# Performance work log

Hardware: AMD Instinct MI355X
Metric: run time of the kernel (lower is better)

The kernel has to match this reference:

```python
import jax, jax.numpy as jnp
import numpy as np

N, E, G = 50000, 800000, 64
NODE_DIM, HID, HEADS, EDGE_DIM = 128, 256, 4, 2
LAYER_IN = [NODE_DIM, HID, HID]
LAYER_HEADS = [HEADS, HEADS, 1]
BN_EPS = 1e-5


def setup_inputs() -> dict:
    key = jax.random.key(0)
    ks = iter(jax.random.split(key, 80))
    def nrm(shape, s=0.05):
        return jax.random.normal(next(ks), shape, jnp.float32) * s
    inp = {}
    inp['x'] = jax.random.normal(next(ks), (N, NODE_DIM), jnp.float32)
    inp['edge_index'] = jax.random.randint(next(ks), (2, E), 0, N, jnp.int32)
    inp['edge_attr'] = jax.random.normal(next(ks), (E, EDGE_DIM), jnp.float32)
    inp['batch'] = jnp.sort(jax.random.randint(next(ks), (N,), 0, G, jnp.int32))
    for i in range(3):
        H = LAYER_HEADS[i]; C = HID // H
        inp[f'W{i}'] = nrm((LAYER_IN[i], H * C))
        inp[f'asrc{i}'] = nrm((H, C))
        inp[f'adst{i}'] = nrm((H, C))
        inp[f'We{i}'] = nrm((EDGE_DIM, H * C))
        inp[f'aedge{i}'] = nrm((H, C))
        inp[f'bconv{i}'] = jnp.zeros((HID,), jnp.float32)
        inp[f'bn{i}_g'] = jnp.ones((HID,), jnp.float32)
        inp[f'bn{i}_b'] = jnp.zeros((HID,), jnp.float32)
        inp[f'bn{i}_m'] = nrm((HID,), 0.01)
        inp[f'bn{i}_v'] = jnp.ones((HID,), jnp.float32)
    inp['Wskip'] = nrm((NODE_DIM, HID))
    inp['bskip'] = jnp.zeros((HID,), jnp.float32)
    inp['Wp1'] = nrm((2 * HID, HID))
    inp['bp1'] = jnp.zeros((HID,), jnp.float32)
    inp['Wp2'] = nrm((HID, 1))
    inp['bp2'] = jnp.zeros((1,), jnp.float32)
    return inp


def gat_conv(x, src, dst, ea, W, a_s, a_d, We, a_e, b, H, concat):
    n = x.shape[0]
    C = W.shape[1] // H
    h = (x @ W).reshape(n, H, C)                      # [N,H,C]
    # attention logits per edge (src/dst node terms + edge term)
    al = ((h * a_s).sum(-1)[src]
          + (h * a_d).sum(-1)[dst]
          + ((ea @ We).reshape(-1, H, C) * a_e).sum(-1))  # [Et,H]
    al = jax.nn.leaky_relu(al, 0.2)
    # segment softmax over destination nodes
    amax = jax.ops.segment_max(al, dst, num_segments=n)
    ex = jnp.exp(al - amax[dst])
    den = jax.ops.segment_sum(ex, dst, num_segments=n)
    alpha = ex / (den[dst] + 1e-16)
    out = jax.ops.segment_sum(h[src] * alpha[..., None], dst, num_segments=n)  # [N,H,C]
    out = out.reshape(n, H * C) if concat else out.mean(axis=1)
    return out + b


def _forward(x, edge_index, edge_attr, batch, layer_params, Wskip, bskip, Wp1, bp1, Wp2, bp2):
    n = x.shape[0]
    # add self-loops (PyG GATConv default), edge_attr filled with mean
    loop = jnp.arange(n, dtype=edge_index.dtype)
    src = jnp.concatenate([edge_index[0], loop])
    dst = jnp.concatenate([edge_index[1], loop])
    ea = jnp.concatenate([edge_attr, jnp.broadcast_to(edge_attr.mean(0), (n, edge_attr.shape[1]))], axis=0)
    identity = x
    for i, (W, a_s, a_d, We, a_e, b, g, be, rm, rv) in enumerate(layer_params):
        layer_identity = (identity @ Wskip + bskip) if i == 0 else identity
        concat = i < 2
        H = LAYER_HEADS[i]
        h = gat_conv(x, src, dst, ea, W, a_s, a_d, We, a_e, b, H, concat)
        h = (h - rm) * jax.lax.rsqrt(rv + BN_EPS) * g + be   # BatchNorm1d (eval)
        h = jax.nn.elu(h)
        x = h + layer_identity
        identity = x
    # global mean + max pool per graph
    counts = jnp.maximum(jax.ops.segment_sum(jnp.ones((n,), x.dtype), batch, num_segments=G), 1.0)
    mean_pool = jax.ops.segment_sum(x, batch, num_segments=G) / counts[:, None]
    max_pool = jax.ops.segment_max(x, batch, num_segments=G)
    emb = jnp.concatenate([mean_pool, max_pool], axis=1)      # [G, 2*HID]
    hmid = jax.nn.relu(emb @ Wp1 + bp1)
    return hmid @ Wp2 + bp2                                   # [G, 1]


def reference(x, edge_index, edge_attr, batch,
              W0, asrc0, adst0, We0, aedge0, bconv0, bn0_g, bn0_b, bn0_m, bn0_v,
              W1, asrc1, adst1, We1, aedge1, bconv1, bn1_g, bn1_b, bn1_m, bn1_v,
              W2, asrc2, adst2, We2, aedge2, bconv2, bn2_g, bn2_b, bn2_m, bn2_v,
              Wskip, bskip, Wp1, bp1, Wp2, bp2):
    layer_params = [
        (W0, asrc0, adst0, We0, aedge0, bconv0, bn0_g, bn0_b, bn0_m, bn0_v),
        (W1, asrc1, adst1, We1, aedge1, bconv1, bn1_g, bn1_b, bn1_m, bn1_v),
        (W2, asrc2, adst2, We2, aedge2, bconv2, bn2_g, bn2_b, bn2_m, bn2_v),
    ]
    return _forward(x, edge_index, edge_attr, batch, layer_params, Wskip, bskip, Wp1, bp1, Wp2, bp2)
```

## Files before the change

### kernel.cpp

```cpp
#include <hip/hip_runtime.h>
#include <cfloat>

#define Nn 50000
#define Ee 800000
#define Etot (Ee + Nn)
#define Gg 64
#define HIDc 256
#define BN_EPS 1e-5f

typedef unsigned int   uint32;
typedef unsigned short ushort16;
typedef short  bf16x8 __attribute__((ext_vector_type(8)));
typedef float  f32x4  __attribute__((ext_vector_type(4)));

__device__ inline ushort16 f2bf(float f) {
    uint32 u = __float_as_uint(f);
    u = (u + 0x7fffu + ((u >> 16) & 1u)) >> 16;
    return (ushort16)u;
}
__device__ inline uint32 pack2(float a, float b) {
    return (uint32)f2bf(a) | ((uint32)f2bf(b) << 16);
}
__device__ inline uint32 fenc(float f) {
    uint32 b = __float_as_uint(f);
    return (b & 0x80000000u) ? ~b : (b | 0x80000000u);
}
__device__ inline float fdec(uint32 u) {
    uint32 b = (u & 0x80000000u) ? (u & 0x7fffffffu) : ~u;
    return __uint_as_float(b);
}

__device__ inline long ws_index(int c, int k, int KB) {
    int cb = c >> 4, m = c & 15, kb = k >> 5, q = (k >> 3) & 3, e = k & 7;
    return (((long)(cb * KB + kb) * 64 + q * 16 + m) << 3) + e;
}

#define CVT4 (Nn * 128 / 4)
#define CVT_BLKS ((CVT4 + 255) / 256)
#define EBKS ((Etot + 255) / 256)
__global__ __launch_bounds__(256) void prep_kernel(
        const float* __restrict__ ea, float* __restrict__ ea_s,
        const float* __restrict__ We0, const float* __restrict__ ae0,
        const float* __restrict__ We1, const float* __restrict__ ae1,
        const float* __restrict__ We2, const float* __restrict__ ae2,
        float* __restrict__ M,
        const float* __restrict__ W0, const float* __restrict__ Wskip,
        const float* __restrict__ W1, const float* __restrict__ W2,
        ushort16* __restrict__ WtC, ushort16* __restrict__ Wt1,
        ushort16* __restrict__ Wt2,
        const float* __restrict__ x, ushort16* __restrict__ xbf,
        const int* __restrict__ ei, int* __restrict__ counts) {
    int bid = blockIdx.x, t = threadIdx.x;
    if (bid < 256) {
        __shared__ float sh0[256], sh1[256];
        float s0 = 0.f, s1 = 0.f;
        for (int e = bid * 256 + t; e < Ee; e += 256 * 256) {
            s0 += ea[2 * e];
            s1 += ea[2 * e + 1];
        }
        sh0[t] = s0; sh1[t] = s1;
        __syncthreads();
        for (int off = 128; off > 0; off >>= 1) {
            if (t < off) { sh0[t] += sh0[t + off]; sh1[t] += sh1[t + off]; }
            __syncthreads();
        }
        if (t == 0) { atomicAdd(&ea_s[0], sh0[0]); atomicAdd(&ea_s[1], sh1[0]); }
    } else if (bid == 256) {
        if (t >= 18) return;
        int l = t < 8 ? 0 : (t < 16 ? 1 : 2);
        int r = t - l * 8;
        const float* We = (l == 0) ? We0 : (l == 1 ? We1 : We2);
        const float* ae = (l == 0) ? ae0 : (l == 1 ? ae1 : ae2);
        int Hl = (l < 2) ? 4 : 1;
        int Cl = 256 / Hl;
        int d = r / Hl, hh = r % Hl;
        float s = 0.f;
        for (int c = 0; c < Cl; ++c)
            s += We[d * 256 + hh * Cl + c] * ae[hh * Cl + c];
        M[l * 8 + r] = s;
    } else if (bid < 385) {
        int k = bid - 257;
        WtC[ws_index(t, k, 4)] = f2bf(W0[(long)k * 256 + t]);
    } else if (bid < 513) {
        int k = bid - 385;
        WtC[ws_index(256 + t, k, 4)] = f2bf(Wskip[(long)k * 256 + t]);
    } else if (bid < 769) {
        int k = bid - 513;
        Wt1[ws_index(t, k, 8)] = f2bf(W1[(long)k * 256 + t]);
    } else if (bid < 1025) {
        int k = bid - 769;
        Wt2[ws_index(t, k, 8)] = f2bf(W2[(long)k * 256 + t]);
    } else if (bid < 1025 + CVT_BLKS) {
        int i = (bid - 1025) * 256 + t;
        if (i < CVT4) {
            float4 v = *(const float4*)&x[i * 4];
            ushort4 o;
            o.x = f2bf(v.x); o.y = f2bf(v.y); o.z = f2bf(v.z); o.w = f2bf(v.w);
            *(ushort4*)&xbf[i * 4] = o;
        }
    } else {
        int e = (bid - 1025 - CVT_BLKS) * 256 + t;
        if (e < Etot) {
            int d = (e < Ee) ? ei[Ee + e] : (e - Ee);
            atomicAdd(&counts[d], 1);
        }
    }
}

__global__ void scan1_kernel(const int* __restrict__ in, int* __restrict__ inc,
                             int* __restrict__ bsums) {
    __shared__ int sh[256];
    int i = blockIdx.x * 256 + threadIdx.x;
    int v = (i < Nn) ? in[i] : 0;
    sh[threadIdx.x] = v;
    __syncthreads();
    for (int off = 1; off < 256; off <<= 1) {
        int t = ((int)threadIdx.x >= off) ? sh[threadIdx.x - off] : 0;
        __syncthreads();
        sh[threadIdx.x] += t;
        __syncthreads();
    }
    if (i < Nn) inc[i] = sh[threadIdx.x];
    if (threadIdx.x == 255) bsums[blockIdx.x] = sh[255];
}

__global__ void scan23_kernel(const int* __restrict__ inc, const int* __restrict__ bsums,
                              int* __restrict__ row_start, int* __restrict__ cursor, int nb) {
    __shared__ int sh[256];
    int b = blockIdx.x, t = threadIdx.x;
    sh[t] = (t < b && t < nb) ? bsums[t] : 0;
    __syncthreads();
    for (int off = 128; off > 0; off >>= 1) {
        if (t < off) sh[t] += sh[t + off];
        __syncthreads();
    }
    int base = sh[0];
    int i = b * 256 + t;
    if (i < Nn) {
        int v = inc[i] + base;
        row_start[i + 1] = v;
        cursor[i + 1] = v;
    }
    if (i == 0) { row_start[0] = 0; cursor[0] = 0; }
}

__global__ void scatter_kernel(const int* __restrict__ ei, const float* __restrict__ ea,
                               const float* __restrict__ ea_sum, int* __restrict__ cursor,
                               int* __restrict__ src_sorted, float* __restrict__ ea_sorted) {
    int e = blockIdx.x * blockDim.x + threadIdx.x;
    if (e >= Etot) return;
    int s, d; float e0, e1;
    if (e < Ee) {
        s = ei[e]; d = ei[Ee + e];
        e0 = ea[2 * e]; e1 = ea[2 * e + 1];
    } else {
        s = d = e - Ee;
        const float invE = 1.f / (float)Ee;
        e0 = ea_sum[0] * invE; e1 = ea_sum[1] * invE;
    }
    int pos = atomicAdd(&cursor[d], 1);
    src_sorted[pos] = s;
    ea_sorted[2 * pos]     = e0;
    ea_sorted[2 * pos + 1] = e1;
}

#define LDK 40
__global__ __launch_bounds__(256) void mfma_gemm_kernel(
        const ushort16* __restrict__ A,
        const ushort16* __restrict__ WS,
        uint32* __restrict__ outF,
        uint32* __restrict__ outS,
        const float* __restrict__ bskip,
        const float* __restrict__ a_s, const float* __restrict__ a_d,
        float* __restrict__ ssrc, float* __restrict__ sdst,
        int n, int K) {
    __shared__ ushort16 As[128 * LDK];
    const int t    = threadIdx.x;
    const int row0 = blockIdx.x * 128;
    const int c0   = blockIdx.y * 128;
    const bool isSkip = (outS != nullptr) && (c0 >= 256);
    const int cc0  = isSkip ? c0 - 256 : c0;
    const int wave = t >> 6, lane = t & 63;
    const int wr = wave >> 1, wc = wave & 1;
    const int l15 = lane & 15, quad = lane >> 4;
    const int KB = K >> 5;

    f32x4 acc[4][4];
#pragma unroll
    for (int j = 0; j < 4; ++j)
#pragma unroll
        for (int i = 0; i < 4; ++i) {
            acc[j][i][0] = 0.f; acc[j][i][1] = 0.f;
            acc[j][i][2] = 0.f; acc[j][i][3] = 0.f;
        }

    const int sm = t & 127;
    const int so = t >> 7;

    for (int k0 = 0; k0 < K; k0 += 32) {
        const int kb = k0 >> 5;
#pragma unroll
        for (int h = 0; h < 2; ++h) {
            int oct = so + 2 * h;
            int grow = row0 + sm;
            uint4 va = make_uint4(0, 0, 0, 0);
            if (grow < n) va = *(const uint4*)&A[(long)grow * K + k0 + 8 * oct];
            *(uint4*)&As[sm * LDK + 8 * oct] = va;
        }
        bf16x8 bfv[4];
#pragma unroll
        for (int j = 0; j < 4; ++j) {
            int cb = ((c0 + wc * 64) >> 4) + j;
            bfv[j] = *(const bf16x8*)&WS[(((long)cb * KB + kb) * 64 + lane) << 3];
        }
        __syncthreads();
        bf16x8 af[4];
#pragma unroll
        for (int i = 0; i < 4; ++i)
            af[i] = *(const bf16x8*)&As[(wr * 64 + i * 16 + l15) * LDK + quad * 8];
#pragma unroll
        for (int j = 0; j < 4; ++j)
#pragma unroll
            for (int i = 0; i < 4; ++i)
                acc[j][i] = __builtin_amdgcn_mfma_f32_16x16x32_bf16(
                    bfv[j], af[i], acc[j][i], 0, 0, 0);
        __syncthreads();
    }

    float4 bb[4];
#pragma unroll
    for (int j = 0; j < 4; ++j) {
        if (isSkip) bb[j] = *(const float4*)&bskip[cc0 + wc * 64 + j * 16 + quad * 4];
        else        bb[j] = make_float4(0.f, 0.f, 0.f, 0.f);
    }

    uint32* tgt = isSkip ? outS : outF;
#pragma unroll
    for (int i = 0; i < 4; ++i) {
        int row = row0 + wr * 64 + i * 16 + l15;
        if (row >= n) continue;
#pragma unroll
        for (int j = 0; j < 4; ++j) {
            int col = cc0 + wc * 64 + j * 16 + quad * 4;
            uint2 pk;
            pk.x = pack2(acc[j][i][0] + bb[j].x, acc[j][i][1] + bb[j].y);
            pk.y = pack2(acc[j][i][2] + bb[j].z, acc[j][i][3] + bb[j].w);
            *(uint2*)&tgt[(long)row * 128 + (col >> 1)] = pk;
        }
    }

    if (!isSkip && a_s != nullptr) {
        float4 asv[4], adv[4];
#pragma unroll
        for (int j = 0; j < 4; ++j) {
            int col = cc0 + wc * 64 + j * 16 + quad * 4;
            asv[j] = *(const float4*)&a_s[col];
            adv[j] = *(const float4*)&a_d[col];
        }
        const int part = (cc0 + wc * 64) >> 6;
#pragma unroll
        for (int i = 0; i < 4; ++i) {
            float ps = 0.f, pd = 0.f;
#pragma unroll
            for (int j = 0; j < 4; ++j) {
                ps += acc[j][i][0] * asv[j].x + acc[j][i][1] * asv[j].y
                    + acc[j][i][2] * asv[j].z + acc[j][i][3] * asv[j].w;
                pd += acc[j][i][0] * adv[j].x + acc[j][i][1] * adv[j].y
                    + acc[j][i][2] * adv[j].z + acc[j][i][3] * adv[j].w;
            }
            ps += __shfl_xor(ps, 16); ps += __shfl_xor(ps, 32);
            pd += __shfl_xor(pd, 16); pd += __shfl_xor(pd, 32);
            if (quad == 0) {
                int row = row0 + wr * 64 + i * 16 + l15;
                if (row < n) {
                    ssrc[row * 4 + part] = ps;
                    sdst[row * 4 + part] = pd;
                }
            }
        }
    }
}

template <int H>
__global__ __launch_bounds__(256) void edge_softmax_kernel(
        const int* __restrict__ src_sorted, const int* __restrict__ row_start,
        const float* __restrict__ ea_sorted, const float* __restrict__ ssrc,
        const float* __restrict__ sdst, const float* __restrict__ M,
        float* __restrict__ w) {
    int node = (blockIdx.x * blockDim.x + threadIdx.x) >> 4;
    int l16 = threadIdx.x & 15;
    if (node >= Nn) return;
    int beg = row_start[node], end = row_start[node + 1];
    int deg = end - beg;
    float sd[H], M0[H], M1[H], m[H], den[H];
    if (H == 4) {
#pragma unroll
        for (int h = 0; h < H; ++h) sd[h] = sdst[node * 4 + h];
    } else {
        float4 v = *(const float4*)&sdst[node * 4];
        sd[0] = v.x + v.y + v.z + v.w;
    }
#pragma unroll
    for (int h = 0; h < H; ++h) {
        M0[h] = M[h]; M1[h] = M[H + h];
        m[h] = -FLT_MAX; den[h] = 0.f;
    }
    auto ssval = [&](int s, int h) -> float {
        if (H == 4) return ssrc[s * 4 + h];
        float4 v = *(const float4*)&ssrc[s * 4];
        return v.x + v.y + v.z + v.w;
    };
    if (deg <= 64) {
        float lreg[4][H];
#pragma unroll
        for (int k = 0; k < 4; ++k) {
            int idx = beg + l16 + (k << 4);
            if (idx < end) {
                int s = src_sorted[idx];
                float e0 = ea_sorted[2 * idx], e1 = ea_sorted[2 * idx + 1];
#pragma unroll
                for (int h = 0; h < H; ++h) {
                    float l = ssval(s, h) + sd[h] + e0 * M0[h] + e1 * M1[h];
                    l = (l > 0.f) ? l : 0.2f * l;
                    lreg[k][h] = l;
                    if (l > m[h]) { den[h] = den[h] * __expf(m[h] - l) + 1.f; m[h] = l; }
                    else den[h] += __expf(l - m[h]);
                }
            }
        }
#pragma unroll
        for (int h = 0; h < H; ++h) {
#pragma unroll
            for (int off = 1; off < 16; off <<= 1) {
                float om = __shfl_xor(m[h], off);
                float od = __shfl_xor(den[h], off);
                float nm = fmaxf(m[h], om);
                den[h] = den[h] * __expf(m[h] - nm) + od * __expf(om - nm);
                m[h] = nm;
            }
            den[h] = 1.f / (den[h] + 1e-16f);
        }
#pragma unroll
        for (int k = 0; k < 4; ++k) {
            int idx = beg + l16 + (k << 4);
            if (idx < end) {
#pragma unroll
                for (int h = 0; h < H; ++h)
                    w[(long)idx * H + h] = __expf(lreg[k][h] - m[h]) * den[h];
            }
        }
    } else {
        for (int idx = beg + l16; idx < end; idx += 16) {
            int s = src_sorted[idx];
            float e0 = ea_sorted[2 * idx], e1 = ea_sorted[2 * idx + 1];
#pragma unroll
            for (int h = 0; h < H; ++h) {
                float l = ssval(s, h) + sd[h] + e0 * M0[h] + e1 * M1[h];
                l = (l > 0.f) ? l : 0.2f * l;
                w[(long)idx * H + h] = l;
                if (l > m[h]) { den[h] = den[h] * __expf(m[h] - l) + 1.f; m[h] = l; }
                else den[h] += __expf(l - m[h]);
            }
        }
#pragma unroll
        for (int h = 0; h < H; ++h) {
#pragma unroll
            for (int off = 1; off < 16; off <<= 1) {
                float om = __shfl_xor(m[h], off);
                float od = __shfl_xor(den[h], off);
                float nm = fmaxf(m[h], om);
                den[h] = den[h] * __expf(m[h] - nm) + od * __expf(om - nm);
                m[h] = nm;
            }
            den[h] = 1.f / (den[h] + 1e-16f);
        }
        for (int idx = beg + l16; idx < end; idx += 16) {
#pragma unroll
            for (int h = 0; h < H; ++h) {
                float l = w[(long)idx * H + h];
                w[(long)idx * H + h] = __expf(l - m[h]) * den[h];
            }
        }
    }
}

template <int H>
__global__ __launch_bounds__(256) void agg_kernel(
        const int* __restrict__ src_sorted, const int* __restrict__ row_start,
        const uint32* __restrict__ hbuf2, const float* __restrict__ w,
        const float* __restrict__ bconv,
        const float* __restrict__ bn_g, const float* __restrict__ bn_b,
        const float* __restrict__ bn_m, const float* __restrict__ bn_v,
        const uint32* __restrict__ identity2, uint32* __restrict__ out2) {
    int wv = threadIdx.x >> 6;
    int l  = threadIdx.x & 63;
    int node = blockIdx.x * 4 + wv;
    if (node >= Nn) return;
    const int hh = (l >> 4) & (H - 1);
    const int l15 = l & 15, gbase = l & 48;
    int beg = row_start[node], end = row_start[node + 1];
    float a0 = 0.f, a1 = 0.f, a2 = 0.f, a3 = 0.f;
    for (int base = beg; base < end; base += 16) {
        int bi  = base + l15;
        int bic = min(bi, end - 1);
        int sp  = src_sorted[bic];
        float wp = (bi < end) ? w[(long)bic * H + hh] : 0.f;
        uint2 f[16];
        float wk[16];
#pragma unroll
        for (int k = 0; k < 16; ++k) {
            int sl = gbase + k;
            int sk = __shfl(sp, sl, 64);
            wk[k]  = __shfl(wp, sl, 64);
            f[k] = *(const uint2*)&hbuf2[(long)sk * 128 + 2 * l];
        }
#pragma unroll
        for (int k = 0; k < 16; ++k) {
            float ww = wk[k];
            a0 += ww * __uint_as_float(f[k].x << 16);
            a1 += ww * __uint_as_float(f[k].x & 0xffff0000u);
            a2 += ww * __uint_as_float(f[k].y << 16);
            a3 += ww * __uint_as_float(f[k].y & 0xffff0000u);
        }
    }
    int c = 4 * l;
    float4 bcv = *(const float4*)&bconv[c];
    float4 bgv = *(const float4*)&bn_g[c];
    float4 bbv = *(const float4*)&bn_b[c];
    float4 bmv = *(const float4*)&bn_m[c];
    float4 bvv = *(const float4*)&bn_v[c];
    float v0 = a0 + bcv.x, v1 = a1 + bcv.y, v2 = a2 + bcv.z, v3 = a3 + bcv.w;
    v0 = (v0 - bmv.x) * rsqrtf(bvv.x + BN_EPS) * bgv.x + bbv.x;
    v1 = (v1 - bmv.y) * rsqrtf(bvv.y + BN_EPS) * bgv.y + bbv.y;
    v2 = (v2 - bmv.z) * rsqrtf(bvv.z + BN_EPS) * bgv.z + bbv.z;
    v3 = (v3 - bmv.w) * rsqrtf(bvv.w + BN_EPS) * bgv.w + bbv.w;
    v0 = (v0 > 0.f) ? v0 : (expf(v0) - 1.f);
    v1 = (v1 > 0.f) ? v1 : (expf(v1) - 1.f);
    v2 = (v2 > 0.f) ? v2 : (expf(v2) - 1.f);
    v3 = (v3 > 0.f) ? v3 : (expf(v3) - 1.f);
    uint2 idu = *(const uint2*)&identity2[(long)node * 128 + 2 * l];
    v0 += __uint_as_float(idu.x << 16);
    v1 += __uint_as_float(idu.x & 0xffff0000u);
    v2 += __uint_as_float(idu.y << 16);
    v3 += __uint_as_float(idu.y & 0xffff0000u);
    uint2 o;
    o.x = pack2(v0, v1);
    o.y = pack2(v2, v3);
    *(uint2*)&out2[(long)node * 128 + 2 * l] = o;
}

#define POOL_ROWS 32
__global__ __launch_bounds__(128) void pool_kernel(
        const uint32* __restrict__ x2, const int* __restrict__ batch,
        float* __restrict__ psum, uint32* __restrict__ pmax, float* __restrict__ pcnt) {
    int c2 = threadIdx.x;
    int n0 = blockIdx.x * POOL_ROWS;
    if (n0 >= Nn) return;
    int n1 = min(n0 + POOL_ROWS, Nn);
    int cur = batch[n0];
    float s0 = 0.f, s1 = 0.f, m0 = -FLT_MAX, m1 = -FLT_MAX;
    int cnt = 0;
    int c = 2 * c2;
    for (int i = n0; i < n1; ++i) {
        int g = batch[i];
        if (g != cur) {
            atomicAdd(&psum[cur * 256 + c], s0);
            atomicAdd(&psum[cur * 256 + c + 1], s1);
            atomicMax(&pmax[cur * 256 + c], fenc(m0));
            atomicMax(&pmax[cur * 256 + c + 1], fenc(m1));
            if (c2 == 0) atomicAdd(&pcnt[cur], (float)cnt);
            cur = g; s0 = s1 = 0.f; m0 = m1 = -FLT_MAX; cnt = 0;
        }
        uint32 u = x2[(long)i * 128 + c2];
        float lo = __uint_as_float(u << 16);
        float hi = __uint_as_float(u & 0xffff0000u);
        s0 += lo; s1 += hi;
        m0 = fmaxf(m0, lo); m1 = fmaxf(m1, hi);
        ++cnt;
    }
    atomicAdd(&psum[cur * 256 + c], s0);
    atomicAdd(&psum[cur * 256 + c + 1], s1);
    atomicMax(&pmax[cur * 256 + c], fenc(m0));
    atomicMax(&pmax[cur * 256 + c + 1], fenc(m1));
    if (c2 == 0) atomicAdd(&pcnt[cur], (float)cnt);
}

__global__ __launch_bounds__(256) void mlp_kernel(
        const float* __restrict__ psum, const uint32* __restrict__ pmax,
        const float* __restrict__ pcnt, const float* __restrict__ Wp1,
        const float* __restrict__ bp1, const float* __restrict__ Wp2,
        const float* __restrict__ bp2, float* __restrict__ out) {
    int g = blockIdx.x;
    int j = threadIdx.x;
    float inv = 1.f / fmaxf(pcnt[g], 1.f);
    float acc = bp1[j];
    for (int k = 0; k < 256; ++k)
        acc += (psum[g * 256 + k] * inv) * Wp1[k * 256 + j];
    for (int k = 0; k < 256; ++k)
        acc += fdec(pmax[g * 256 + k]) * Wp1[(256 + k) * 256 + j];
    float v = fmaxf(acc, 0.f) * Wp2[j];
    __shared__ float red[256];
    red[j] = v;
    __syncthreads();
    for (int off = 128; off > 0; off >>= 1) {
        if (j < off) red[j] += red[j + off];
        __syncthreads();
    }
    if (j == 0) out[g] = red[0] + bp2[0];
}

extern "C" void kernel_launch(void* const* d_in, const int* in_sizes, int n_in,
                              void* d_out, int out_size, void* d_ws, size_t ws_size,
                              hipStream_t stream) {
    const float* x   = (const float*)d_in[0];
    const int*   ei  = (const int*)d_in[1];
    const float* ea  = (const float*)d_in[2];
    const int*   bat = (const int*)d_in[3];
    auto LP = [&](int l, int j) { return (const float*)d_in[4 + l * 10 + j]; };
    const float* Wskip = (const float*)d_in[34];
    const float* bskip = (const float*)d_in[35];
    const float* Wp1   = (const float*)d_in[36];
    const float* bp1   = (const float*)d_in[37];
    const float* Wp2   = (const float*)d_in[38];
    const float* bp2   = (const float*)d_in[39];
    float* out = (float*)d_out;

    char* p = (char*)d_ws;
    auto alloc = [&](size_t bytes) { void* r = (void*)p; p += (bytes + 255) & ~(size_t)255; return r; };
    uint32*   hbuf2  = (uint32*)alloc((size_t)Nn * 256 * 2);
    uint32*   skipbf = (uint32*)alloc((size_t)Nn * 128 * 4);
    uint32*   resA   = (uint32*)alloc((size_t)Nn * 128 * 4);
    uint32*   resB   = (uint32*)alloc((size_t)Nn * 128 * 4);
    ushort16* xbf    = (ushort16*)alloc((size_t)Nn * 128 * 2);
    float*    wbuf   = (float*)alloc((size_t)Etot * 4 * 4);
    float*    ea_sorted = (float*)alloc((size_t)Etot * 2 * 4);
    float*    ssrc   = (float*)alloc((size_t)Nn * 4 * 4);
    float*    sdst   = (float*)alloc((size_t)Nn * 4 * 4);
    int*      counts = (int*)alloc((size_t)Nn * 4);
    int*      incb   = (int*)alloc((size_t)Nn * 4);
    int*      row_start = (int*)alloc((size_t)(Nn + 1) * 4);
    int*      cursor    = (int*)alloc((size_t)(Nn + 1) * 4);
    int*      src_sorted = (int*)alloc((size_t)Etot * 4);
    int*      bsums  = (int*)alloc(256 * 4);
    float*    ea_s   = (float*)alloc(2 * 4);
    float*    Mbuf   = (float*)alloc(32 * 4);
    ushort16* WtC    = (ushort16*)alloc((size_t)512 * 128 * 2);
    ushort16* Wt1    = (ushort16*)alloc((size_t)256 * 256 * 2);
    ushort16* Wt2    = (ushort16*)alloc((size_t)256 * 256 * 2);
    float*    psum   = (float*)alloc((size_t)Gg * 256 * 4);
    uint32*   pmax   = (uint32*)alloc((size_t)Gg * 256 * 4);
    float*    pcnt   = (float*)alloc((size_t)Gg * 4);

    const int nb = (Nn + 255) / 256;
    const int sgrid = (Nn * 16 + 255) / 256;

    hipMemsetAsync(counts, 0, (size_t)Nn * 4, stream);
    hipMemsetAsync(ea_s, 0, 8, stream);
    hipMemsetAsync(psum, 0, (size_t)Gg * 256 * 4 * 2 + (size_t)Gg * 4, stream);

    prep_kernel<<<1025 + CVT_BLKS + EBKS, 256, 0, stream>>>(
        ea, ea_s, LP(0,3), LP(0,4), LP(1,3), LP(1,4), LP(2,3), LP(2,4), Mbuf,
        LP(0,0), Wskip, LP(1,0), LP(2,0), WtC, Wt1, Wt2, x, xbf, ei, counts);

    scan1_kernel<<<nb, 256, 0, stream>>>(counts, incb, bsums);
    scan23_kernel<<<nb, 256, 0, stream>>>(incb, bsums, row_start, cursor, nb);
    scatter_kernel<<<EBKS, 256, 0, stream>>>(ei, ea, ea_s, cursor, src_sorted, ea_sorted);

    {
        dim3 g0((Nn + 127) / 128, 4);
        mfma_gemm_kernel<<<g0, 256, 0, stream>>>(
            xbf, WtC, hbuf2, skipbf, bskip,
            LP(0,1), LP(0,2), ssrc, sdst, Nn, 128);
    }

    const uint32* lid[3] = { skipbf, resA, resB };
    uint32*       lou[3] = { resA, resB, resA };
    const ushort16* lain[3] = { nullptr, (ushort16*)resA, (ushort16*)resB };
    const ushort16* lwt[3]  = { nullptr, Wt1, Wt2 };
    for (int l = 0; l < 3; ++l) {
        if (l > 0) {
            dim3 gl((Nn + 127) / 128, 2);
            mfma_gemm_kernel<<<gl, 256, 0, stream>>>(
                lain[l], lwt[l], hbuf2, nullptr, nullptr,
                LP(l,1), LP(l,2), ssrc, sdst, Nn, 256);
        }
        if (l < 2) {
            edge_softmax_kernel<4><<<sgrid, 256, 0, stream>>>(
                src_sorted, row_start, ea_sorted, ssrc, sdst, Mbuf + l * 8, wbuf);
            agg_kernel<4><<<(Nn + 3) / 4, 256, 0, stream>>>(src_sorted, row_start, hbuf2, wbuf,
                LP(l,5), LP(l,6), LP(l,7), LP(l,8), LP(l,9), lid[l], lou[l]);
        } else {
            edge_softmax_kernel<1><<<sgrid, 256, 0, stream>>>(
                src_sorted, row_start, ea_sorted, ssrc, sdst, Mbuf + l * 8, wbuf);
            agg_kernel<1><<<(Nn + 3) / 4, 256, 0, stream>>>(src_sorted, row_start, hbuf2, wbuf,
                LP(l,5), LP(l,6), LP(l,7), LP(l,8), LP(l,9), lid[l], lou[l]);
        }
    }

    pool_kernel<<<(Nn + POOL_ROWS - 1) / POOL_ROWS, 128, 0, stream>>>(resA, bat, psum, pmax, pcnt);
    mlp_kernel<<<Gg, 256, 0, stream>>>(psum, pmax, pcnt, Wp1, bp1, Wp2, bp2, out);
}
```

Baseline: 643.7 us.

## Fuse edge softmax into the aggregation kernel using per-wave shared memory

```diff
diff --git a/kernel.cpp b/kernel.cpp
--- a/kernel.cpp
+++ b/kernel.cpp
@@ -282,147 +282,144 @@
 }
 
 template <int H>
-__global__ __launch_bounds__(256) void edge_softmax_kernel(
+__global__ __launch_bounds__(256) void agg_fused_kernel(
         const int* __restrict__ src_sorted, const int* __restrict__ row_start,
         const float* __restrict__ ea_sorted, const float* __restrict__ ssrc,
         const float* __restrict__ sdst, const float* __restrict__ M,
-        float* __restrict__ w) {
-    int node = (blockIdx.x * blockDim.x + threadIdx.x) >> 4;
-    int l16 = threadIdx.x & 15;
-    if (node >= Nn) return;
-    int beg = row_start[node], end = row_start[node + 1];
-    int deg = end - beg;
-    float sd[H], M0[H], M1[H], m[H], den[H];
-    if (H == 4) {
-#pragma unroll
-        for (int h = 0; h < H; ++h) sd[h] = sdst[node * 4 + h];
-    } else {
-        float4 v = *(const float4*)&sdst[node * 4];
-        sd[0] = v.x + v.y + v.z + v.w;
-    }
-#pragma unroll
-    for (int h = 0; h < H; ++h) {
-        M0[h] = M[h]; M1[h] = M[H + h];
-        m[h] = -FLT_MAX; den[h] = 0.f;
-    }
-    auto ssval = [&](int s, int h) -> float {
-        if (H == 4) return ssrc[s * 4 + h];
-        float4 v = *(const float4*)&ssrc[s * 4];
-        return v.x + v.y + v.z + v.w;
-    };
-    if (deg <= 64) {
-        float lreg[4][H];
-#pragma unroll
-        for (int k = 0; k < 4; ++k) {
-            int idx = beg + l16 + (k << 4);
-            if (idx < end) {
-                int s = src_sorted[idx];
-                float e0 = ea_sorted[2 * idx], e1 = ea_sorted[2 * idx + 1];
-#pragma unroll
-                for (int h = 0; h < H; ++h) {
-                    float l = ssval(s, h) + sd[h] + e0 * M0[h] + e1 * M1[h];
-                    l = (l > 0.f) ? l : 0.2f * l;
-                    lreg[k][h] = l;
-                    if (l > m[h]) { den[h] = den[h] * __expf(m[h] - l) + 1.f; m[h] = l; }
-                    else den[h] += __expf(l - m[h]);
-                }
-            }
-        }
-#pragma unroll
-        for (int h = 0; h < H; ++h) {
-#pragma unroll
-            for (int off = 1; off < 16; off <<= 1) {
-                float om = __shfl_xor(m[h], off);
-                float od = __shfl_xor(den[h], off);
-                float nm = fmaxf(m[h], om);
-                den[h] = den[h] * __expf(m[h] - nm) + od * __expf(om - nm);
-                m[h] = nm;
-            }
-            den[h] = 1.f / (den[h] + 1e-16f);
-        }
-#pragma unroll
-        for (int k = 0; k < 4; ++k) {
-            int idx = beg + l16 + (k << 4);
-            if (idx < end) {
-#pragma unroll
-                for (int h = 0; h < H; ++h)
-                    w[(long)idx * H + h] = __expf(lreg[k][h] - m[h]) * den[h];
-            }
-        }
-    } else {
-        for (int idx = beg + l16; idx < end; idx += 16) {
-            int s = src_sorted[idx];
-            float e0 = ea_sorted[2 * idx], e1 = ea_sorted[2 * idx + 1];
-#pragma unroll
-            for (int h = 0; h < H; ++h) {
-                float l = ssval(s, h) + sd[h] + e0 * M0[h] + e1 * M1[h];
-                l = (l > 0.f) ? l : 0.2f * l;
-                w[(long)idx * H + h] = l;
-                if (l > m[h]) { den[h] = den[h] * __expf(m[h] - l) + 1.f; m[h] = l; }
-                else den[h] += __expf(l - m[h]);
-            }
-        }
-#pragma unroll
-        for (int h = 0; h < H; ++h) {
-#pragma unroll
-            for (int off = 1; off < 16; off <<= 1) {
-                float om = __shfl_xor(m[h], off);
-                float od = __shfl_xor(den[h], off);
-                float nm = fmaxf(m[h], om);
-                den[h] = den[h] * __expf(m[h] - nm) + od * __expf(om - nm);
-                m[h] = nm;
-            }
-            den[h] = 1.f / (den[h] + 1e-16f);
-        }
-        for (int idx = beg + l16; idx < end; idx += 16) {
-#pragma unroll
-            for (int h = 0; h < H; ++h) {
-                float l = w[(long)idx * H + h];
-                w[(long)idx * H + h] = __expf(l - m[h]) * den[h];
-            }
-        }
-    }
-}
-
-template <int H>
-__global__ __launch_bounds__(256) void agg_kernel(
-        const int* __restrict__ src_sorted, const int* __restrict__ row_start,
-        const uint32* __restrict__ hbuf2, const float* __restrict__ w,
+        const uint32* __restrict__ hbuf2,
         const float* __restrict__ bconv,
         const float* __restrict__ bn_g, const float* __restrict__ bn_b,
         const float* __restrict__ bn_m, const float* __restrict__ bn_v,
-        const uint32* __restrict__ identity2, uint32* __restrict__ out2) {
-    int wv = threadIdx.x >> 6;
-    int l  = threadIdx.x & 63;
-    int node = blockIdx.x * 4 + wv;
+        const uint32* __restrict__ identity2, uint32* __restrict__ out2,
+        float* __restrict__ wspill) {
+    __shared__ int   s_sh[4][64];
+    __shared__ float w_sh[4][64 * H];
+    const int wv = threadIdx.x >> 6;
+    const int l  = threadIdx.x & 63;
+    const int node = blockIdx.x * 4 + wv;
     if (node >= Nn) return;
-    const int hh = (l >> 4) & (H - 1);
-    const int l15 = l & 15, gbase = l & 48;
-    int beg = row_start[node], end = row_start[node + 1];
+    const int hh = (H == 4) ? (l >> 4) : 0;
+    const int beg = row_start[node], end = row_start[node + 1];
+    const int deg = end - beg;
+
+    float M0[H], M1[H], sd[H];
+    {
+        float4 sdv = *(const float4*)&sdst[node * 4];
+        if (H == 4) { sd[0] = sdv.x; sd[1] = sdv.y; sd[2] = sdv.z; sd[3] = sdv.w; }
+        else         sd[0] = sdv.x + sdv.y + sdv.z + sdv.w;
+#pragma unroll
+        for (int h = 0; h < H; ++h) { M0[h] = M[h]; M1[h] = M[H + h]; }
+    }
+
     float a0 = 0.f, a1 = 0.f, a2 = 0.f, a3 = 0.f;
-    for (int base = beg; base < end; base += 16) {
-        int bi  = base + l15;
-        int bic = min(bi, end - 1);
-        int sp  = src_sorted[bic];
-        float wp = (bi < end) ? w[(long)bic * H + hh] : 0.f;
-        uint2 f[16];
-        float wk[16];
-#pragma unroll
-        for (int k = 0; k < 16; ++k) {
-            int sl = gbase + k;
-            int sk = __shfl(sp, sl, 64);
-            wk[k]  = __shfl(wp, sl, 64);
-            f[k] = *(const uint2*)&hbuf2[(long)sk * 128 + 2 * l];
-        }
-#pragma unroll
-        for (int k = 0; k < 16; ++k) {
-            float ww = wk[k];
-            a0 += ww * __uint_as_float(f[k].x << 16);
-            a1 += ww * __uint_as_float(f[k].x & 0xffff0000u);
-            a2 += ww * __uint_as_float(f[k].y << 16);
-            a3 += ww * __uint_as_float(f[k].y & 0xffff0000u);
-        }
-    }
+
+    auto gather = [&](int cnt) {
+        for (int base = 0; base < cnt; base += 16) {
+            int sk[16]; float wk[16]; uint2 f[16];
+#pragma unroll
+            for (int k = 0; k < 16; ++k) {
+                sk[k] = s_sh[wv][base + k];
+                wk[k] = w_sh[wv][(base + k) * H + hh];
+            }
+#pragma unroll
+            for (int k = 0; k < 16; ++k)
+                f[k] = *(const uint2*)&hbuf2[(long)sk[k] * 128 + 2 * l];
+#pragma unroll
+            for (int k = 0; k < 16; ++k) {
+                float ww = wk[k];
+                a0 += ww * __uint_as_float(f[k].x << 16);
+                a1 += ww * __uint_as_float(f[k].x & 0xffff0000u);
+                a2 += ww * __uint_as_float(f[k].y << 16);
+                a3 += ww * __uint_as_float(f[k].y & 0xffff0000u);
+            }
+        }
+    };
+
+    if (deg <= 64) {
+        const int  el  = beg + l;
+        const bool act = l < deg;
+        const int  elc = min(el, end - 1);
+        const int  s   = src_sorted[elc];
+        const float e0 = ea_sorted[2 * elc], e1 = ea_sorted[2 * elc + 1];
+        float4 sv = *(const float4*)&ssrc[s * 4];
+        float lh[H], m[H], dn[H];
+#pragma unroll
+        for (int h = 0; h < H; ++h) {
+            float ss = (H == 4) ? ((const float*)&sv)[h]
+                                : (sv.x + sv.y + sv.z + sv.w);
+            float lg = ss + sd[h] + e0 * M0[h] + e1 * M1[h];
+            lg = (lg > 0.f) ? lg : 0.2f * lg;
+            lh[h] = lg;
+            m[h]  = act ? lg : -FLT_MAX;
+            dn[h] = act ? 1.f : 0.f;
+        }
+#pragma unroll
+        for (int h = 0; h < H; ++h) {
+#pragma unroll
+            for (int off = 1; off < 64; off <<= 1) {
+                float om = __shfl_xor(m[h], off, 64);
+                float od = __shfl_xor(dn[h], off, 64);
+                float nm = fmaxf(m[h], om);
+                dn[h] = dn[h] * __expf(m[h] - nm) + od * __expf(om - nm);
+                m[h] = nm;
+            }
+            dn[h] = 1.f / (dn[h] + 1e-16f);
+        }
+        s_sh[wv][l] = s;
+#pragma unroll
+        for (int h = 0; h < H; ++h)
+            w_sh[wv][l * H + h] = act ? __expf(lh[h] - m[h]) * dn[h] : 0.f;
+        asm volatile("s_waitcnt lgkmcnt(0)" ::: "memory");
+        gather(deg);
+    } else {
+        float m[H], dn[H];
+#pragma unroll
+        for (int h = 0; h < H; ++h) { m[h] = -FLT_MAX; dn[h] = 0.f; }
+        for (int cb = beg; cb < end; cb += 64) {
+            int el = cb + l; bool act = el < end;
+            int elc = min(el, end - 1);
+            int s = src_sorted[elc];
+            float e0 = ea_sorted[2 * elc], e1 = ea_sorted[2 * elc + 1];
+            float4 sv = *(const float4*)&ssrc[s * 4];
+#pragma unroll
+            for (int h = 0; h < H; ++h) {
+                float ss = (H == 4) ? ((const float*)&sv)[h]
+                                    : (sv.x + sv.y + sv.z + sv.w);
+                float lg = ss + sd[h] + e0 * M0[h] + e1 * M1[h];
+                lg = (lg > 0.f) ? lg : 0.2f * lg;
+                if (act) {
+                    wspill[(long)el * H + h] = lg;
+                    if (lg > m[h]) { dn[h] = dn[h] * __expf(m[h] - lg) + 1.f; m[h] = lg; }
+                    else dn[h] += __expf(lg - m[h]);
+                }
+            }
+        }
+#pragma unroll
+        for (int h = 0; h < H; ++h) {
+#pragma unroll
+            for (int off = 1; off < 64; off <<= 1) {
+                float om = __shfl_xor(m[h], off, 64);
+                float od = __shfl_xor(dn[h], off, 64);
+                float nm = fmaxf(m[h], om);
+                dn[h] = dn[h] * __expf(m[h] - nm) + od * __expf(om - nm);
+                m[h] = nm;
+            }
+            dn[h] = 1.f / (dn[h] + 1e-16f);
+        }
+        for (int cb = beg; cb < end; cb += 64) {
+            int el = cb + l; bool act = el < end;
+            int elc = min(el, end - 1);
+            s_sh[wv][l] = src_sorted[elc];
+#pragma unroll
+            for (int h = 0; h < H; ++h)
+                w_sh[wv][l * H + h] =
+                    act ? __expf(wspill[(long)el * H + h] - m[h]) * dn[h] : 0.f;
+            asm volatile("s_waitcnt lgkmcnt(0)" ::: "memory");
+            gather(min(64, end - cb));
+            asm volatile("s_waitcnt lgkmcnt(0)" ::: "memory");
+        }
+    }
+
     int c = 4 * l;
     float4 bcv = *(const float4*)&bconv[c];
     float4 bgv = *(const float4*)&bn_g[c];
@@ -552,7 +549,6 @@
     float*    pcnt   = (float*)alloc((size_t)Gg * 4);
 
     const int nb = (Nn + 255) / 256;
-    const int sgrid = (Nn * 16 + 255) / 256;
 
     hipMemsetAsync(counts, 0, (size_t)Nn * 4, stream);
     hipMemsetAsync(ea_s, 0, 8, stream);
@@ -584,17 +580,16 @@
                 lain[l], lwt[l], hbuf2, nullptr, nullptr,
                 LP(l,1), LP(l,2), ssrc, sdst, Nn, 256);
         }
-        if (l < 2) {
-            edge_softmax_kernel<4><<<sgrid, 256, 0, stream>>>(
-                src_sorted, row_start, ea_sorted, ssrc, sdst, Mbuf + l * 8, wbuf);
-            agg_kernel<4><<<(Nn + 3) / 4, 256, 0, stream>>>(src_sorted, row_start, hbuf2, wbuf,
-                LP(l,5), LP(l,6), LP(l,7), LP(l,8), LP(l,9), lid[l], lou[l]);
-        } else {
-            edge_softmax_kernel<1><<<sgrid, 256, 0, stream>>>(
-                src_sorted, row_start, ea_sorted, ssrc, sdst, Mbuf + l * 8, wbuf);
-            agg_kernel<1><<<(Nn + 3) / 4, 256, 0, stream>>>(src_sorted, row_start, hbuf2, wbuf,
-                LP(l,5), LP(l,6), LP(l,7), LP(l,8), LP(l,9), lid[l], lou[l]);
-        }
+        if (l < 2)
+            agg_fused_kernel<4><<<(Nn + 3) / 4, 256, 0, stream>>>(
+                src_sorted, row_start, ea_sorted, ssrc, sdst, Mbuf + l * 8,
+                hbuf2, LP(l,5), LP(l,6), LP(l,7), LP(l,8), LP(l,9),
+                lid[l], lou[l], wbuf);
+        else
+            agg_fused_kernel<1><<<(Nn + 3) / 4, 256, 0, stream>>>(
+                src_sorted, row_start, ea_sorted, ssrc, sdst, Mbuf + l * 8,
+                hbuf2, LP(l,5), LP(l,6), LP(l,7), LP(l,8), LP(l,9),
+                lid[l], lou[l], wbuf);
     }
 
     pool_kernel<<<(Nn + POOL_ROWS - 1) / POOL_ROWS, 128, 0, stream>>>(resA, bat, psum, pmax, pcnt);
```

Result: no change. 635.2 us (-1.3%).
